# Kernel optimization log

Hardware: AMD Instinct MI355X
Metric: run time of the kernel (lower is better)

Reference implementation:

```python
import jax, jax.numpy as jnp
import numpy as np
import math

D_MODEL = 1024
HEADS = 16
HEAD_DIM = D_MODEL // HEADS
BATCH = 2
SEQ = 2048


def setup_inputs() -> dict:
    key = jax.random.key(0)
    ks = jax.random.split(key, 6)
    scale = 1.0 / math.sqrt(D_MODEL)
    return {
        "x": jax.random.normal(ks[0], (BATCH, SEQ, D_MODEL), dtype=jnp.float32),
        "mask": jnp.zeros((SEQ, SEQ), dtype=jnp.float32),
        "w_qkv": jax.random.normal(ks[1], (D_MODEL, 3 * D_MODEL), dtype=jnp.float32) * scale,
        "b_qkv": jax.random.normal(ks[2], (3 * D_MODEL,), dtype=jnp.float32) * 0.01,
        "w_out": jax.random.normal(ks[3], (D_MODEL, D_MODEL), dtype=jnp.float32) * scale,
        "b_out": jax.random.normal(ks[4], (D_MODEL,), dtype=jnp.float32) * 0.01,
    }


def reference(x, mask, w_qkv, b_qkv, w_out, b_out):
    B, S, D = x.shape
    H, hd = HEADS, HEAD_DIM
    # fused QKV projection: [B,S,3D]
    qkv = x @ w_qkv + b_qkv
    # [B,S,H,3*hd] -> [B,H,S,3*hd]
    qkv = qkv.reshape(B, S, H, 3 * hd).transpose(0, 2, 1, 3)
    q, k, v = jnp.split(qkv, 3, axis=-1)  # each [B,H,S,hd]
    inv_sqrt_d = jnp.asarray(1.0 / math.sqrt(hd), dtype=x.dtype)
    scores = jnp.einsum("bhqd,bhkd->bhqk", q, k) * inv_sqrt_d
    # additive mask; [S,S] broadcasts identically in [H,B,S,S] or [B,H,S,S] layout
    scores = scores + mask
    attn = jax.nn.softmax(scores, axis=-1)
    vals = jnp.einsum("bhqk,bhkd->bhqd", attn, v)  # [B,H,S,hd]
    vals = vals.transpose(0, 2, 1, 3).reshape(B, S, H * hd)
    return vals @ w_out + b_out
```

## Files before the change

kernel.cpp:

```cpp
#include <hip/hip_runtime.h>


typedef __bf16 bf16;
typedef __bf16 bf16x2 __attribute__((ext_vector_type(2)));
typedef __bf16 bf16x4 __attribute__((ext_vector_type(4)));
typedef __bf16 bf16x8 __attribute__((ext_vector_type(8)));
typedef float f32x4 __attribute__((ext_vector_type(4)));

#define MFMA(a, b, c) __builtin_amdgcn_mfma_f32_16x16x32_bf16((a), (b), (c), 0, 0, 0)

#if __has_builtin(__builtin_amdgcn_exp2f)
#define EXP2(x) __builtin_amdgcn_exp2f(x)
#else
#define EXP2(x) exp2f(x)
#endif

__device__ __forceinline__ void load_lds16(const bf16* g, void* l) {
    __builtin_amdgcn_global_load_lds(
        (const __attribute__((address_space(1))) unsigned int*)g,
        (__attribute__((address_space(3))) unsigned int*)l, 16, 0, 0);
}

__global__ void cast4_kernel(const float* __restrict__ in, bf16* __restrict__ out, int n4) {
    int i = blockIdx.x * blockDim.x + threadIdx.x;
    if (i < n4) {
        float4 v = ((const float4*)in)[i];
        bf16x4 o = {(bf16)v.x, (bf16)v.y, (bf16)v.z, (bf16)v.w};
        ((bf16x4*)out)[i] = o;
    }
}

__global__ void transpose_cast_kernel(const float* __restrict__ in, bf16* __restrict__ out,
                                      int R, int C) {
    __shared__ float tile[32][33];
    int bx = blockIdx.x * 32;
    int by = blockIdx.y * 32;
    int tx = threadIdx.x, ty = threadIdx.y;
    for (int i = 0; i < 32; i += 8)
        tile[ty + i][tx] = in[(size_t)(by + ty + i) * C + bx + tx];
    __syncthreads();
    for (int i = 0; i < 32; i += 8)
        out[(size_t)(bx + ty + i) * R + by + tx] = (bf16)tile[tx][ty + i];
}

__global__ __launch_bounds__(256) void gemm_qkv_kernel(
    const bf16* __restrict__ A, const bf16* __restrict__ BT,
    const float* __restrict__ bias,
    bf16* __restrict__ Q, bf16* __restrict__ K, bf16* __restrict__ VT) {
    __shared__ __attribute__((aligned(16))) char lds[2][16384];
    int bm = blockIdx.x, bn = blockIdx.y;
    int t = threadIdx.x;
    int w = t >> 6, lane = t & 63, g = lane >> 4, l16 = lane & 15;
    int wm = (w >> 1) * 64, wn = (w & 1) * 64;
    f32x4 acc[4][4] = {};
    const bf16* Ablk = A + (size_t)(bm * 128) * 1024;
    const bf16* Bblk = BT + (size_t)(bn * 128) * 1024;
    int srow = t >> 2;
    int scg = (t & 3) ^ (srow & 3);
    const bf16* ag0 = Ablk + (size_t)srow * 1024 + scg * 8;
    const bf16* ag1 = ag0 + 64 * 1024;
    const bf16* bg0 = Bblk + (size_t)srow * 1024 + scg * 8;
    const bf16* bg1 = bg0 + 64 * 1024;

    load_lds16(ag0, lds[0] + t * 16);
    load_lds16(ag1, lds[0] + 4096 + t * 16);
    load_lds16(bg0, lds[0] + 8192 + t * 16);
    load_lds16(bg1, lds[0] + 12288 + t * 16);
    asm volatile("s_waitcnt vmcnt(0)" ::: "memory");

    int sw = l16 & 3;
#pragma unroll 2
    for (int j = 0; j < 32; j++) {
        asm volatile("s_barrier" ::: "memory");
        int jp = j + 1 < 32 ? j + 1 : 31;
        char* dst = lds[(j + 1) & 1];
        load_lds16(ag0 + jp * 32, dst + t * 16);
        load_lds16(ag1 + jp * 32, dst + 4096 + t * 16);
        load_lds16(bg0 + jp * 32, dst + 8192 + t * 16);
        load_lds16(bg1 + jp * 32, dst + 12288 + t * 16);

        const bf16* As = (const bf16*)lds[j & 1];
        const bf16* Bs = (const bf16*)(lds[j & 1] + 8192);
        bf16x8 af[4], bfr[4];
#pragma unroll
        for (int mi = 0; mi < 4; mi++) {
            int row = wm + mi * 16 + l16;
            af[mi] = *(const bf16x8*)(&As[row * 32 + (g ^ sw) * 8]);
        }
#pragma unroll
        for (int ni = 0; ni < 4; ni++) {
            int row = wn + ni * 16 + l16;
            bfr[ni] = *(const bf16x8*)(&Bs[row * 32 + (g ^ sw) * 8]);
        }
#pragma unroll
        for (int mi = 0; mi < 4; mi++)
#pragma unroll
            for (int ni = 0; ni < 4; ni++)
                acc[mi][ni] = MFMA(bfr[ni], af[mi], acc[mi][ni]);
        asm volatile("s_waitcnt vmcnt(0)" ::: "memory");
    }
    __syncthreads();

    bf16* vt = (bf16*)lds;
    int b = bm >> 4;
    int row0 = (bm & 15) * 128 + wm;
    int half_col = bn * 128 + wn;
    int h = half_col / 192, tt = half_col % 192;
    size_t bh = (size_t)(b * 16 + h);

    if (tt < 128) {
        bf16* base = (tt == 0 ? Q : K) + bh * 2048 * 64;
#pragma unroll
        for (int mi = 0; mi < 4; mi++) {
#pragma unroll
            for (int ni = 0; ni < 4; ni++) {
                int d0 = ni * 16 + g * 4;
                float4 bv = *(const float4*)(&bias[half_col + d0]);
                int s = row0 + mi * 16 + l16;
                bf16x4 pk = {(bf16)(acc[mi][ni][0] + bv.x), (bf16)(acc[mi][ni][1] + bv.y),
                             (bf16)(acc[mi][ni][2] + bv.z), (bf16)(acc[mi][ni][3] + bv.w)};
                *(bf16x4*)(&base[(size_t)s * 64 + d0]) = pk;
            }
        }
    } else {
#pragma unroll
        for (int mi = 0; mi < 4; mi++) {
            int s_local = wm + mi * 16 + l16;
#pragma unroll
            for (int ni = 0; ni < 4; ni++) {
                int d0 = ni * 16 + g * 4;
                float4 bv = *(const float4*)(&bias[half_col + d0]);
                vt[(d0 + 0) * 136 + s_local] = (bf16)(acc[mi][ni][0] + bv.x);
                vt[(d0 + 1) * 136 + s_local] = (bf16)(acc[mi][ni][1] + bv.y);
                vt[(d0 + 2) * 136 + s_local] = (bf16)(acc[mi][ni][2] + bv.z);
                vt[(d0 + 3) * 136 + s_local] = (bf16)(acc[mi][ni][3] + bv.w);
            }
        }
    }
    __syncthreads();

    int hc0 = bn * 128, hc1 = bn * 128 + 64;
    int vhalf = (hc0 % 192 == 128) ? 0 : ((hc1 % 192 == 128) ? 1 : -1);
    if (vhalf >= 0) {
        int vcol = bn * 128 + vhalf * 64;
        size_t vbh = (size_t)(b * 16 + vcol / 192);
        int d = t >> 2, ch = t & 3;
        const bf16* src = &vt[d * 136 + ch * 32];
        bf16* dstp = &VT[(vbh * 64 + d) * 2048 + (bm & 15) * 128 + ch * 32];
#pragma unroll
        for (int k = 0; k < 4; k++)
            *(bf16x8*)(&dstp[k * 8]) = *(const bf16x8*)(&src[k * 8]);
    }
}

__global__ __launch_bounds__(256) void gemm_out_kernel(
    const bf16* __restrict__ A, const bf16* __restrict__ BT,
    const float* __restrict__ bias, float* __restrict__ out) {
    __shared__ __attribute__((aligned(16))) char lds[2][12288];
    int bm = blockIdx.x, bn = blockIdx.y;
    int t = threadIdx.x;
    int w = t >> 6, lane = t & 63, g = lane >> 4, l16 = lane & 15;
    int wm = (w >> 1) * 64, wn = (w & 1) * 32;
    f32x4 acc[4][2] = {};
    const bf16* Ablk = A + (size_t)(bm * 128) * 1024;
    const bf16* Bblk = BT + (size_t)(bn * 64) * 1024;
    int srow = t >> 2;
    int scg = (t & 3) ^ (srow & 3);
    const bf16* ag0 = Ablk + (size_t)srow * 1024 + scg * 8;
    const bf16* ag1 = ag0 + 64 * 1024;
    const bf16* bg0 = Bblk + (size_t)srow * 1024 + scg * 8;

    load_lds16(ag0, lds[0] + t * 16);
    load_lds16(ag1, lds[0] + 4096 + t * 16);
    load_lds16(bg0, lds[0] + 8192 + t * 16);
    asm volatile("s_waitcnt vmcnt(0)" ::: "memory");

    int sw = l16 & 3;
#pragma unroll 2
    for (int j = 0; j < 32; j++) {
        asm volatile("s_barrier" ::: "memory");
        int jp = j + 1 < 32 ? j + 1 : 31;
        char* dst = lds[(j + 1) & 1];
        load_lds16(ag0 + jp * 32, dst + t * 16);
        load_lds16(ag1 + jp * 32, dst + 4096 + t * 16);
        load_lds16(bg0 + jp * 32, dst + 8192 + t * 16);

        const bf16* As = (const bf16*)lds[j & 1];
        const bf16* Bs = (const bf16*)(lds[j & 1] + 8192);
        bf16x8 af[4], bfr[2];
#pragma unroll
        for (int mi = 0; mi < 4; mi++) {
            int row = wm + mi * 16 + l16;
            af[mi] = *(const bf16x8*)(&As[row * 32 + (g ^ sw) * 8]);
        }
#pragma unroll
        for (int ni = 0; ni < 2; ni++) {
            int row = wn + ni * 16 + l16;
            bfr[ni] = *(const bf16x8*)(&Bs[row * 32 + (g ^ sw) * 8]);
        }
#pragma unroll
        for (int mi = 0; mi < 4; mi++)
#pragma unroll
            for (int ni = 0; ni < 2; ni++)
                acc[mi][ni] = MFMA(bfr[ni], af[mi], acc[mi][ni]);
        asm volatile("s_waitcnt vmcnt(0)" ::: "memory");
    }

#pragma unroll
    for (int mi = 0; mi < 4; mi++) {
#pragma unroll
        for (int ni = 0; ni < 2; ni++) {
            int row = bm * 128 + wm + mi * 16 + l16;
            int col0 = bn * 64 + wn + ni * 16 + g * 4;
            float4 bv = *(const float4*)(&bias[col0]);
            float4 ov = {acc[mi][ni][0] + bv.x, acc[mi][ni][1] + bv.y,
                         acc[mi][ni][2] + bv.z, acc[mi][ni][3] + bv.w};
            *(float4*)(&out[(size_t)row * 1024 + col0]) = ov;
        }
    }
}

__global__ __launch_bounds__(256, 2) void attn_kernel(
    const bf16* __restrict__ Q, const bf16* __restrict__ K,
    const bf16* __restrict__ VT, const float* __restrict__ mask,
    bf16* __restrict__ vals) {
    __shared__ __attribute__((aligned(16))) char lds[4][8192];

    int blk = blockIdx.x;
    int bh = ((blk & 7) << 2) | ((blk >> 3) & 3);
    int qt = blk >> 5;
    int t = threadIdx.x;
    int w = t >> 6, lane = t & 63, g = lane >> 4, l16 = lane & 15;
    int qw = qt * 128 + w * 32;

    const bf16* Qp = Q + (size_t)bh * 2048 * 64;
    const bf16* Kp = K + (size_t)bh * 2048 * 64;
    const bf16* Vp = VT + (size_t)bh * 64 * 2048;
    const float* mrowA = mask + (size_t)(qw + l16) * 2048;
    const float* mrowB = mask + (size_t)(qw + 16 + l16) * 2048;

    int ks_row = t >> 3;
    int ks_cblk = (t & 7) ^ (ks_row & 7);
    const bf16* kg = Kp + ks_row * 64 + ks_cblk * 8;
    int vs_d = t >> 2;
    int vs_sblk = (t & 3) ^ ((t >> 3) & 3);
    const bf16* vg = Vp + (size_t)vs_d * 2048 + vs_sblk * 8;

    const float SCL = 0.125f * 1.44269504089f;
    const float L2E = 1.44269504089f;

    bf16x8 qa0 = *(const bf16x8*)(&Qp[(size_t)(qw + l16) * 64 + g * 8]);
    bf16x8 qa1 = *(const bf16x8*)(&Qp[(size_t)(qw + l16) * 64 + 32 + g * 8]);
    bf16x8 qb0 = *(const bf16x8*)(&Qp[(size_t)(qw + 16 + l16) * 64 + g * 8]);
    bf16x8 qb1 = *(const bf16x8*)(&Qp[(size_t)(qw + 16 + l16) * 64 + 32 + g * 8]);
    load_lds16(kg + 0, &lds[0][t * 16]);
    load_lds16(vg + 0, &lds[0][4096 + t * 16]);
    float4 mva0 = *(const float4*)(&mrowA[0 + g * 4]);
    float4 mva1 = *(const float4*)(&mrowA[16 + g * 4]);
    float4 mvb0 = *(const float4*)(&mrowB[0 + g * 4]);
    float4 mvb1 = *(const float4*)(&mrowB[16 + g * 4]);
    load_lds16(kg + 1 * 32 * 64, &lds[1][t * 16]);
    load_lds16(vg + 1 * 32, &lds[1][4096 + t * 16]);
    asm volatile("s_waitcnt vmcnt(0)" ::: "memory");
    asm volatile("s_barrier" ::: "memory");

    f32x4 o[4][2] = {};
    float la = 0.f, lb = 0.f;

    for (int j = 0; j < 64; j++) {
        int buf = j & 3;
        int jm = j + 1 < 64 ? j + 1 : 63;
        float4 nmva0 = *(const float4*)(&mrowA[jm * 32 + g * 4]);
        float4 nmva1 = *(const float4*)(&mrowA[jm * 32 + 16 + g * 4]);
        float4 nmvb0 = *(const float4*)(&mrowB[jm * 32 + g * 4]);
        float4 nmvb1 = *(const float4*)(&mrowB[jm * 32 + 16 + g * 4]);
        int jp = j + 2 < 64 ? j + 2 : 63;
        load_lds16(kg + (size_t)jp * 32 * 64, &lds[(j + 2) & 3][t * 16]);
        load_lds16(vg + jp * 32, &lds[(j + 2) & 3][4096 + t * 16]);
        asm volatile("s_waitcnt vmcnt(12)" ::: "memory");
        asm volatile("s_barrier" ::: "memory");

        float pa[8], pb[8];
#pragma unroll
        for (int ts = 0; ts < 2; ts++) {
            int s0 = ts * 16 + l16;
            int swz = s0 & 7;
            bf16x8 k0 = *(const bf16x8*)(&lds[buf][(s0 * 8 + (g ^ swz)) * 16]);
            bf16x8 k1 = *(const bf16x8*)(&lds[buf][(s0 * 8 + ((4 + g) ^ swz)) * 16]);
            f32x4 sta = {}, stb = {};
            sta = MFMA(k0, qa0, sta);
            sta = MFMA(k1, qa1, sta);
            stb = MFMA(k0, qb0, stb);
            stb = MFMA(k1, qb1, stb);
            float4 ma = ts ? mva1 : mva0;
            float4 mb = ts ? mvb1 : mvb0;
            pa[ts * 4 + 0] = EXP2(sta[0] * SCL + ma.x * L2E);
            pa[ts * 4 + 1] = EXP2(sta[1] * SCL + ma.y * L2E);
            pa[ts * 4 + 2] = EXP2(sta[2] * SCL + ma.z * L2E);
            pa[ts * 4 + 3] = EXP2(sta[3] * SCL + ma.w * L2E);
            pb[ts * 4 + 0] = EXP2(stb[0] * SCL + mb.x * L2E);
            pb[ts * 4 + 1] = EXP2(stb[1] * SCL + mb.y * L2E);
            pb[ts * 4 + 2] = EXP2(stb[2] * SCL + mb.z * L2E);
            pb[ts * 4 + 3] = EXP2(stb[3] * SCL + mb.w * L2E);
        }
#pragma unroll
        for (int i = 0; i < 8; i++) { la += pa[i]; lb += pb[i]; }

        int selA = (((2 * g) & 3) << 4) | l16;
        int selB = (((2 * g + 1) & 3) << 4) | l16;
        bool hi = (g & 2) != 0;
        union { int i[4]; bf16x8 v; } pua, pub;
        {
            union { bf16x2 h; int i; } u;
            int dw0, dw1, dw2, dw3;
            u.h = bf16x2{(bf16)pa[0], (bf16)pa[1]}; dw0 = u.i;
            u.h = bf16x2{(bf16)pa[2], (bf16)pa[3]}; dw1 = u.i;
            u.h = bf16x2{(bf16)pa[4], (bf16)pa[5]}; dw2 = u.i;
            u.h = bf16x2{(bf16)pa[6], (bf16)pa[7]}; dw3 = u.i;
            int t0a = __shfl(dw0, selA, 64), t2a = __shfl(dw2, selA, 64);
            int t1a = __shfl(dw1, selA, 64), t3a = __shfl(dw3, selA, 64);
            int t0b = __shfl(dw0, selB, 64), t2b = __shfl(dw2, selB, 64);
            int t1b = __shfl(dw1, selB, 64), t3b = __shfl(dw3, selB, 64);
            pua.i[0] = hi ? t2a : t0a;
            pua.i[1] = hi ? t3a : t1a;
            pua.i[2] = hi ? t2b : t0b;
            pua.i[3] = hi ? t3b : t1b;
        }
        {
            union { bf16x2 h; int i; } u;
            int dw0, dw1, dw2, dw3;
            u.h = bf16x2{(bf16)pb[0], (bf16)pb[1]}; dw0 = u.i;
            u.h = bf16x2{(bf16)pb[2], (bf16)pb[3]}; dw1 = u.i;
            u.h = bf16x2{(bf16)pb[4], (bf16)pb[5]}; dw2 = u.i;
            u.h = bf16x2{(bf16)pb[6], (bf16)pb[7]}; dw3 = u.i;
            int t0a = __shfl(dw0, selA, 64), t2a = __shfl(dw2, selA, 64);
            int t1a = __shfl(dw1, selA, 64), t3a = __shfl(dw3, selA, 64);
            int t0b = __shfl(dw0, selB, 64), t2b = __shfl(dw2, selB, 64);
            int t1b = __shfl(dw1, selB, 64), t3b = __shfl(dw3, selB, 64);
            pub.i[0] = hi ? t2a : t0a;
            pub.i[1] = hi ? t3a : t1a;
            pub.i[2] = hi ? t2b : t0b;
            pub.i[3] = hi ? t3b : t1b;
        }

#pragma unroll
        for (int nc = 0; nc < 4; nc++) {
            int d = nc * 16 + l16;
            int slot = d * 4 + (g ^ ((d >> 1) & 3));
            bf16x8 vf = *(const bf16x8*)(&lds[buf][4096 + slot * 16]);
            o[nc][0] = MFMA(vf, pua.v, o[nc][0]);
            o[nc][1] = MFMA(vf, pub.v, o[nc][1]);
        }

        mva0 = nmva0; mva1 = nmva1;
        mvb0 = nmvb0; mvb1 = nmvb1;
    }
    asm volatile("s_waitcnt vmcnt(0)" ::: "memory");

    la += __shfl_xor(la, 16, 64);
    la += __shfl_xor(la, 32, 64);
    lb += __shfl_xor(lb, 16, 64);
    lb += __shfl_xor(lb, 32, 64);
    int b = bh >> 4, h = bh & 15;
    float lia = 1.f / la, lib = 1.f / lb;
    size_t rowA = (size_t)(b * 2048 + qw + l16);
    size_t rowB = rowA + 16;
#pragma unroll
    for (int nc = 0; nc < 4; nc++) {
        bf16x4 pkA = {(bf16)(o[nc][0][0] * lia), (bf16)(o[nc][0][1] * lia),
                      (bf16)(o[nc][0][2] * lia), (bf16)(o[nc][0][3] * lia)};
        *(bf16x4*)(&vals[rowA * 1024 + h * 64 + nc * 16 + g * 4]) = pkA;
        bf16x4 pkB = {(bf16)(o[nc][1][0] * lib), (bf16)(o[nc][1][1] * lib),
                      (bf16)(o[nc][1][2] * lib), (bf16)(o[nc][1][3] * lib)};
        *(bf16x4*)(&vals[rowB * 1024 + h * 64 + nc * 16 + g * 4]) = pkB;
    }
}

extern "C" void kernel_launch(void* const* d_in, const int* in_sizes, int n_in,
                              void* d_out, int out_size, void* d_ws, size_t ws_size,
                              hipStream_t stream) {
    const float* x     = (const float*)d_in[0];
    const float* mask  = (const float*)d_in[1];
    const float* w_qkv = (const float*)d_in[2];
    const float* b_qkv = (const float*)d_in[3];
    const float* w_out = (const float*)d_in[4];
    const float* b_out = (const float*)d_in[5];
    float* out = (float*)d_out;

    char* ws = (char*)d_ws;
    size_t off = 0;
    bf16* xb    = (bf16*)(ws + off); off += (size_t)4096 * 1024 * 2;
    bf16* wqkvT = (bf16*)(ws + off); off += (size_t)3072 * 1024 * 2;
    bf16* woutT = (bf16*)(ws + off); off += (size_t)1024 * 1024 * 2;
    bf16* Qa    = (bf16*)(ws + off); off += (size_t)32 * 2048 * 64 * 2;
    bf16* Ka    = (bf16*)(ws + off); off += (size_t)32 * 2048 * 64 * 2;
    bf16* VTa   = (bf16*)(ws + off); off += (size_t)32 * 64 * 2048 * 2;
    bf16* vals  = (bf16*)(ws + off); off += (size_t)4096 * 1024 * 2;

    cast4_kernel<<<4096, 256, 0, stream>>>(x, xb, 4096 * 1024 / 4);
    transpose_cast_kernel<<<dim3(96, 32), dim3(32, 8), 0, stream>>>(w_qkv, wqkvT, 1024, 3072);
    transpose_cast_kernel<<<dim3(32, 32), dim3(32, 8), 0, stream>>>(w_out, woutT, 1024, 1024);
    gemm_qkv_kernel<<<dim3(32, 24), 256, 0, stream>>>(xb, wqkvT, b_qkv, Qa, Ka, VTa);
    attn_kernel<<<512, 256, 0, stream>>>(Qa, Ka, VTa, mask, vals);
    gemm_out_kernel<<<dim3(32, 16), 256, 0, stream>>>(vals, woutT, b_out, out);
}
```

Baseline: 232.8 us.

## Pre-transpose scaled mask and stage GEMM tiles through registers

A new kernel transposes the additive mask and premultiplies it by log2(e), so each attention lane reads mask values along the query index, with neighbouring lanes touching consecutive addresses. The per-element scaling multiply is removed from the softmax inner loop. Both GEMMs replace direct global-to-LDS loads with register-staged loads prefetched two K steps ahead, then written to the double-buffered LDS. The change costs an extra 16MB mask pass and scalar 4-byte mask loads (16 per iteration instead of 4 float4), and the register staging adds VGPR pressure.

```diff
diff --git a/kernel.cpp b/kernel.cpp
--- a/kernel.cpp
+++ b/kernel.cpp
@@ -41,6 +41,19 @@
     __syncthreads();
     for (int i = 0; i < 32; i += 8)
         out[(size_t)(bx + ty + i) * R + by + tx] = (bf16)tile[tx][ty + i];
+}
+
+__global__ void transpose_scale_kernel(const float* __restrict__ in, float* __restrict__ out) {
+    __shared__ float tile[32][33];
+    const float L2E = 1.44269504089f;
+    int bx = blockIdx.x * 32;
+    int by = blockIdx.y * 32;
+    int tx = threadIdx.x, ty = threadIdx.y;
+    for (int i = 0; i < 32; i += 8)
+        tile[ty + i][tx] = in[(size_t)(by + ty + i) * 2048 + bx + tx];
+    __syncthreads();
+    for (int i = 0; i < 32; i += 8)
+        out[(size_t)(bx + ty + i) * 2048 + by + tx] = tile[tx][ty + i] * L2E;
 }
 
 __global__ __launch_bounds__(256) void gemm_qkv_kernel(
@@ -62,22 +75,36 @@
     const bf16* bg0 = Bblk + (size_t)srow * 1024 + scg * 8;
     const bf16* bg1 = bg0 + 64 * 1024;
 
-    load_lds16(ag0, lds[0] + t * 16);
-    load_lds16(ag1, lds[0] + 4096 + t * 16);
-    load_lds16(bg0, lds[0] + 8192 + t * 16);
-    load_lds16(bg1, lds[0] + 12288 + t * 16);
+    bf16x8 ra0 = *(const bf16x8*)(ag0);
+    bf16x8 ra1 = *(const bf16x8*)(ag1);
+    bf16x8 rb0 = *(const bf16x8*)(bg0);
+    bf16x8 rb1 = *(const bf16x8*)(bg1);
     asm volatile("s_waitcnt vmcnt(0)" ::: "memory");
+    *(bf16x8*)(lds[0] + t * 16) = ra0;
+    *(bf16x8*)(lds[0] + 4096 + t * 16) = ra1;
+    *(bf16x8*)(lds[0] + 8192 + t * 16) = rb0;
+    *(bf16x8*)(lds[0] + 12288 + t * 16) = rb1;
+    ra0 = *(const bf16x8*)(ag0 + 32);
+    ra1 = *(const bf16x8*)(ag1 + 32);
+    rb0 = *(const bf16x8*)(bg0 + 32);
+    rb1 = *(const bf16x8*)(bg1 + 32);
 
     int sw = l16 & 3;
 #pragma unroll 2
     for (int j = 0; j < 32; j++) {
+        asm volatile("s_waitcnt lgkmcnt(0)" ::: "memory");
         asm volatile("s_barrier" ::: "memory");
-        int jp = j + 1 < 32 ? j + 1 : 31;
+        asm volatile("s_waitcnt vmcnt(0)" ::: "memory");
         char* dst = lds[(j + 1) & 1];
-        load_lds16(ag0 + jp * 32, dst + t * 16);
-        load_lds16(ag1 + jp * 32, dst + 4096 + t * 16);
-        load_lds16(bg0 + jp * 32, dst + 8192 + t * 16);
-        load_lds16(bg1 + jp * 32, dst + 12288 + t * 16);
+        *(bf16x8*)(dst + t * 16) = ra0;
+        *(bf16x8*)(dst + 4096 + t * 16) = ra1;
+        *(bf16x8*)(dst + 8192 + t * 16) = rb0;
+        *(bf16x8*)(dst + 12288 + t * 16) = rb1;
+        int jp = j + 2 < 32 ? j + 2 : 31;
+        ra0 = *(const bf16x8*)(ag0 + jp * 32);
+        ra1 = *(const bf16x8*)(ag1 + jp * 32);
+        rb0 = *(const bf16x8*)(bg0 + jp * 32);
+        rb1 = *(const bf16x8*)(bg1 + jp * 32);
 
         const bf16* As = (const bf16*)lds[j & 1];
         const bf16* Bs = (const bf16*)(lds[j & 1] + 8192);
@@ -97,7 +124,6 @@
 #pragma unroll
             for (int ni = 0; ni < 4; ni++)
                 acc[mi][ni] = MFMA(bfr[ni], af[mi], acc[mi][ni]);
-        asm volatile("s_waitcnt vmcnt(0)" ::: "memory");
     }
     __syncthreads();
 
@@ -170,20 +196,31 @@
     const bf16* ag1 = ag0 + 64 * 1024;
     const bf16* bg0 = Bblk + (size_t)srow * 1024 + scg * 8;
 
-    load_lds16(ag0, lds[0] + t * 16);
-    load_lds16(ag1, lds[0] + 4096 + t * 16);
-    load_lds16(bg0, lds[0] + 8192 + t * 16);
+    bf16x8 ra0 = *(const bf16x8*)(ag0);
+    bf16x8 ra1 = *(const bf16x8*)(ag1);
+    bf16x8 rb0 = *(const bf16x8*)(bg0);
     asm volatile("s_waitcnt vmcnt(0)" ::: "memory");
+    *(bf16x8*)(lds[0] + t * 16) = ra0;
+    *(bf16x8*)(lds[0] + 4096 + t * 16) = ra1;
+    *(bf16x8*)(lds[0] + 8192 + t * 16) = rb0;
+    ra0 = *(const bf16x8*)(ag0 + 32);
+    ra1 = *(const bf16x8*)(ag1 + 32);
+    rb0 = *(const bf16x8*)(bg0 + 32);
 
     int sw = l16 & 3;
 #pragma unroll 2
     for (int j = 0; j < 32; j++) {
+        asm volatile("s_waitcnt lgkmcnt(0)" ::: "memory");
         asm volatile("s_barrier" ::: "memory");
-        int jp = j + 1 < 32 ? j + 1 : 31;
+        asm volatile("s_waitcnt vmcnt(0)" ::: "memory");
         char* dst = lds[(j + 1) & 1];
-        load_lds16(ag0 + jp * 32, dst + t * 16);
-        load_lds16(ag1 + jp * 32, dst + 4096 + t * 16);
-        load_lds16(bg0 + jp * 32, dst + 8192 + t * 16);
+        *(bf16x8*)(dst + t * 16) = ra0;
+        *(bf16x8*)(dst + 4096 + t * 16) = ra1;
+        *(bf16x8*)(dst + 8192 + t * 16) = rb0;
+        int jp = j + 2 < 32 ? j + 2 : 31;
+        ra0 = *(const bf16x8*)(ag0 + jp * 32);
+        ra1 = *(const bf16x8*)(ag1 + jp * 32);
+        rb0 = *(const bf16x8*)(bg0 + jp * 32);
 
         const bf16* As = (const bf16*)lds[j & 1];
         const bf16* Bs = (const bf16*)(lds[j & 1] + 8192);
@@ -203,7 +240,6 @@
 #pragma unroll
             for (int ni = 0; ni < 2; ni++)
                 acc[mi][ni] = MFMA(bfr[ni], af[mi], acc[mi][ni]);
-        asm volatile("s_waitcnt vmcnt(0)" ::: "memory");
     }
 
 #pragma unroll
@@ -222,7 +258,7 @@
 
 __global__ __launch_bounds__(256, 2) void attn_kernel(
     const bf16* __restrict__ Q, const bf16* __restrict__ K,
-    const bf16* __restrict__ VT, const float* __restrict__ mask,
+    const bf16* __restrict__ VT, const float* __restrict__ maskT,
     bf16* __restrict__ vals) {
     __shared__ __attribute__((aligned(16))) char lds[4][8192];
 
@@ -232,12 +268,11 @@
     int t = threadIdx.x;
     int w = t >> 6, lane = t & 63, g = lane >> 4, l16 = lane & 15;
     int qw = qt * 128 + w * 32;
+    int qA = qw + l16, qB = qw + 16 + l16;
 
     const bf16* Qp = Q + (size_t)bh * 2048 * 64;
     const bf16* Kp = K + (size_t)bh * 2048 * 64;
     const bf16* Vp = VT + (size_t)bh * 64 * 2048;
-    const float* mrowA = mask + (size_t)(qw + l16) * 2048;
-    const float* mrowB = mask + (size_t)(qw + 16 + l16) * 2048;
 
     int ks_row = t >> 3;
     int ks_cblk = (t & 7) ^ (ks_row & 7);
@@ -247,7 +282,6 @@
     const bf16* vg = Vp + (size_t)vs_d * 2048 + vs_sblk * 8;
 
     const float SCL = 0.125f * 1.44269504089f;
-    const float L2E = 1.44269504089f;
 
     bf16x8 qa0 = *(const bf16x8*)(&Qp[(size_t)(qw + l16) * 64 + g * 8]);
     bf16x8 qa1 = *(const bf16x8*)(&Qp[(size_t)(qw + l16) * 64 + 32 + g * 8]);
@@ -255,10 +289,15 @@
     bf16x8 qb1 = *(const bf16x8*)(&Qp[(size_t)(qw + 16 + l16) * 64 + 32 + g * 8]);
     load_lds16(kg + 0, &lds[0][t * 16]);
     load_lds16(vg + 0, &lds[0][4096 + t * 16]);
-    float4 mva0 = *(const float4*)(&mrowA[0 + g * 4]);
-    float4 mva1 = *(const float4*)(&mrowA[16 + g * 4]);
-    float4 mvb0 = *(const float4*)(&mrowB[0 + g * 4]);
-    float4 mvb1 = *(const float4*)(&mrowB[16 + g * 4]);
+    float mA[8], mB[8];
+#pragma unroll
+    for (int ts = 0; ts < 2; ts++)
+#pragma unroll
+        for (int r = 0; r < 4; r++) {
+            size_t srow = (size_t)(ts * 16 + g * 4 + r) * 2048;
+            mA[ts * 4 + r] = maskT[srow + qA];
+            mB[ts * 4 + r] = maskT[srow + qB];
+        }
     load_lds16(kg + 1 * 32 * 64, &lds[1][t * 16]);
     load_lds16(vg + 1 * 32, &lds[1][4096 + t * 16]);
     asm volatile("s_waitcnt vmcnt(0)" ::: "memory");
@@ -270,14 +309,19 @@
     for (int j = 0; j < 64; j++) {
         int buf = j & 3;
         int jm = j + 1 < 64 ? j + 1 : 63;
-        float4 nmva0 = *(const float4*)(&mrowA[jm * 32 + g * 4]);
-        float4 nmva1 = *(const float4*)(&mrowA[jm * 32 + 16 + g * 4]);
-        float4 nmvb0 = *(const float4*)(&mrowB[jm * 32 + g * 4]);
-        float4 nmvb1 = *(const float4*)(&mrowB[jm * 32 + 16 + g * 4]);
+        float nmA[8], nmB[8];
+#pragma unroll
+        for (int ts = 0; ts < 2; ts++)
+#pragma unroll
+            for (int r = 0; r < 4; r++) {
+                size_t srow = (size_t)(jm * 32 + ts * 16 + g * 4 + r) * 2048;
+                nmA[ts * 4 + r] = maskT[srow + qA];
+                nmB[ts * 4 + r] = maskT[srow + qB];
+            }
         int jp = j + 2 < 64 ? j + 2 : 63;
         load_lds16(kg + (size_t)jp * 32 * 64, &lds[(j + 2) & 3][t * 16]);
         load_lds16(vg + jp * 32, &lds[(j + 2) & 3][4096 + t * 16]);
-        asm volatile("s_waitcnt vmcnt(12)" ::: "memory");
+        asm volatile("s_waitcnt vmcnt(18)" ::: "memory");
         asm volatile("s_barrier" ::: "memory");
 
         float pa[8], pb[8];
@@ -292,16 +336,11 @@
             sta = MFMA(k1, qa1, sta);
             stb = MFMA(k0, qb0, stb);
             stb = MFMA(k1, qb1, stb);
-            float4 ma = ts ? mva1 : mva0;
-            float4 mb = ts ? mvb1 : mvb0;
-            pa[ts * 4 + 0] = EXP2(sta[0] * SCL + ma.x * L2E);
-            pa[ts * 4 + 1] = EXP2(sta[1] * SCL + ma.y * L2E);
-            pa[ts * 4 + 2] = EXP2(sta[2] * SCL + ma.z * L2E);
-            pa[ts * 4 + 3] = EXP2(sta[3] * SCL + ma.w * L2E);
-            pb[ts * 4 + 0] = EXP2(stb[0] * SCL + mb.x * L2E);
-            pb[ts * 4 + 1] = EXP2(stb[1] * SCL + mb.y * L2E);
-            pb[ts * 4 + 2] = EXP2(stb[2] * SCL + mb.z * L2E);
-            pb[ts * 4 + 3] = EXP2(stb[3] * SCL + mb.w * L2E);
+#pragma unroll
+            for (int r = 0; r < 4; r++) {
+                pa[ts * 4 + r] = EXP2(sta[r] * SCL + mA[ts * 4 + r]);
+                pb[ts * 4 + r] = EXP2(stb[r] * SCL + mB[ts * 4 + r]);
+            }
         }
 #pragma unroll
         for (int i = 0; i < 8; i++) { la += pa[i]; lb += pb[i]; }
@@ -352,8 +391,8 @@
             o[nc][1] = MFMA(vf, pub.v, o[nc][1]);
         }
 
-        mva0 = nmva0; mva1 = nmva1;
-        mvb0 = nmvb0; mvb1 = nmvb1;
+#pragma unroll
+        for (int i = 0; i < 8; i++) { mA[i] = nmA[i]; mB[i] = nmB[i]; }
     }
     asm volatile("s_waitcnt vmcnt(0)" ::: "memory");
 
@@ -396,11 +435,13 @@
     bf16* Ka    = (bf16*)(ws + off); off += (size_t)32 * 2048 * 64 * 2;
     bf16* VTa   = (bf16*)(ws + off); off += (size_t)32 * 64 * 2048 * 2;
     bf16* vals  = (bf16*)(ws + off); off += (size_t)4096 * 1024 * 2;
+    float* maskT = (float*)(ws + off); off += (size_t)2048 * 2048 * 4;
 
     cast4_kernel<<<4096, 256, 0, stream>>>(x, xb, 4096 * 1024 / 4);
     transpose_cast_kernel<<<dim3(96, 32), dim3(32, 8), 0, stream>>>(w_qkv, wqkvT, 1024, 3072);
     transpose_cast_kernel<<<dim3(32, 32), dim3(32, 8), 0, stream>>>(w_out, woutT, 1024, 1024);
+    transpose_scale_kernel<<<dim3(64, 64), dim3(32, 8), 0, stream>>>(mask, maskT);
     gemm_qkv_kernel<<<dim3(32, 24), 256, 0, stream>>>(xb, wqkvT, b_qkv, Qa, Ka, VTa);
-    attn_kernel<<<512, 256, 0, stream>>>(Qa, Ka, VTa, mask, vals);
+    attn_kernel<<<512, 256, 0, stream>>>(Qa, Ka, VTa, maskT, vals);
     gemm_out_kernel<<<dim3(32, 16), 256, 0, stream>>>(vals, woutT, b_out, out);
 }
```

After: 245.3 us. 5.4% more time.
